# Performance work log

Measured on AMD Instinct MI355X. Metric: run time of the kernel, lower is better.

The kernel has to match this reference:

```python
import jax, jax.numpy as jnp
import numpy as np

N_ROWS = 4_194_304  # batch rows
N_LAYERS = 30


def setup_inputs() -> dict:
    key = jax.random.key(0)
    k1, k2, k3, k4, k5 = jax.random.split(key, 5)
    x1 = jax.random.normal(k1, (N_ROWS, 1), dtype=jnp.float32)
    x2 = jax.random.normal(k2, (N_ROWS, 5), dtype=jnp.float32)
    # Per-layer params stacked: Linear(5->1) weight [1,5] + bias [1]; Linear(1->5, no bias) weight [5,1]
    W1 = jax.random.normal(k3, (N_LAYERS, 1, 5), dtype=jnp.float32) * (1.0 / np.sqrt(5.0))
    b1 = jax.random.normal(k4, (N_LAYERS, 1), dtype=jnp.float32) * (1.0 / np.sqrt(5.0))
    W2 = jax.random.normal(k5, (N_LAYERS, 5, 1), dtype=jnp.float32)
    return {"x1": x1, "x2": x2, "W1": W1, "b1": b1, "W2": W2}


def reference(x1, x2, W1, b1, W2):
    # Chain of 30 UpDownDoubleResNetBlock blocks:
    #   x1 = x1 + relu(x2) @ W1^T + b1   (Linear(5,1) with bias)
    #   x2 = x2 + relu(x1) @ W2^T        (Linear(1,5) no bias)
    def step(carry, params):
        h1, h2 = carry
        w1, bb1, w2 = params  # [1,5], [1], [5,1]
        h1 = h1 + jax.nn.relu(h2) @ w1.T + bb1  # [N,1]
        h2 = h2 + jax.nn.relu(h1) @ w2.T        # [N,5]
        return (h1, h2), None

    (x1, x2), _ = jax.lax.scan(step, (x1, x2), (W1, b1, W2))
    return (x1, x2)
```

## Files before the change

kernel.cpp:

```cpp
#include <hip/hip_runtime.h>

#define NL 30

typedef float f32x2 __attribute__((ext_vector_type(2)));

static __device__ __forceinline__ f32x2 splat2(float v) { return (f32x2){v, v}; }

__global__ __launch_bounds__(256) void drn_kernel(
    const float* __restrict__ x1, const float* __restrict__ x2,
    const float* __restrict__ W1, const float* __restrict__ b1,
    const float* __restrict__ W2,
    float* __restrict__ o1, float* __restrict__ o2, int nrows)
{
    long t = (long)blockIdx.x * blockDim.x + threadIdx.x;
    long row0 = t * 4;
    if (row0 >= nrows) return;

    float4 h1v = *(const float4*)(x1 + row0);
    float xs[20];
    {
        const float4* px2 = (const float4*)(x2 + row0 * 5);
        #pragma unroll
        for (int i = 0; i < 5; ++i) ((float4*)xs)[i] = px2[i];
    }

    f32x2 h1p[2] = { (f32x2){h1v.x, h1v.y}, (f32x2){h1v.z, h1v.w} };
    f32x2 h2[5][2];
    #pragma unroll
    for (int j = 0; j < 5; ++j) {
        h2[j][0] = (f32x2){xs[0 * 5 + j], xs[1 * 5 + j]};
        h2[j][1] = (f32x2){xs[2 * 5 + j], xs[3 * 5 + j]};
    }

    const f32x2 zero = splat2(0.0f);

    for (int l = 0; l < NL; ++l) {
        float w1r[5], w2r[5];
        #pragma unroll
        for (int j = 0; j < 5; ++j) w1r[j] = W1[l * 5 + j];
        float bb = b1[l];
        #pragma unroll
        for (int j = 0; j < 5; ++j) w2r[j] = W2[l * 5 + j];

        #pragma unroll
        for (int p = 0; p < 2; ++p) {
            f32x2 s = h1p[p] + splat2(bb);
            #pragma unroll
            for (int j = 0; j < 5; ++j)
                s += __builtin_elementwise_max(h2[j][p], zero) * splat2(w1r[j]);
            h1p[p] = s;
            f32x2 rh = __builtin_elementwise_max(s, zero);
            #pragma unroll
            for (int j = 0; j < 5; ++j)
                h2[j][p] += rh * splat2(w2r[j]);
        }
    }

    float ys[20];
    #pragma unroll
    for (int j = 0; j < 5; ++j) {
        ys[0 * 5 + j] = h2[j][0].x;
        ys[1 * 5 + j] = h2[j][0].y;
        ys[2 * 5 + j] = h2[j][1].x;
        ys[3 * 5 + j] = h2[j][1].y;
    }

    *(float4*)(o1 + row0) = make_float4(h1p[0].x, h1p[0].y, h1p[1].x, h1p[1].y);
    float4* po2 = (float4*)(o2 + row0 * 5);
    #pragma unroll
    for (int i = 0; i < 5; ++i) po2[i] = ((float4*)ys)[i];
}

extern "C" void kernel_launch(void* const* d_in, const int* in_sizes, int n_in,
                              void* d_out, int out_size, void* d_ws, size_t ws_size,
                              hipStream_t stream) {
    const float* x1 = (const float*)d_in[0];
    const float* x2 = (const float*)d_in[1];
    const float* W1 = (const float*)d_in[2];
    const float* b1 = (const float*)d_in[3];
    const float* W2 = (const float*)d_in[4];
    int nrows = in_sizes[0];
    float* o1 = (float*)d_out;
    float* o2 = (float*)d_out + nrows;

    int nthreads = nrows / 4;
    int block = 256;
    int grid = (nthreads + block - 1) / block;
    drn_kernel<<<grid, block, 0, stream>>>(x1, x2, W1, b1, W2, o1, o2, nrows);
}
```

Measured before the change: 206.9 us.

## Process eight rows per thread with pre-splatted packed params and explicit FMAs

Each thread now handles eight rows instead of four, which halves the thread count and spreads each per-layer weight load over more work. A small pre-kernel packs W1, b1 and W2 into duplicated float2 pairs in workspace, so the main loop can feed packed FMA directly without splat moves. The inner math uses explicit elementwise FMA, and the layer loop is fully unrolled. The cost is higher register pressure (40+ live floats) and lower occupancy, plus an extra kernel launch.

```diff
diff --git a/kernel.cpp b/kernel.cpp
--- a/kernel.cpp
+++ b/kernel.cpp
@@ -4,71 +4,92 @@
 
 typedef float f32x2 __attribute__((ext_vector_type(2)));
 
-static __device__ __forceinline__ f32x2 splat2(float v) { return (f32x2){v, v}; }
+__global__ void pack_params(const float* __restrict__ W1,
+                            const float* __restrict__ b1,
+                            const float* __restrict__ W2,
+                            f32x2* __restrict__ pw) {
+    int i = blockIdx.x * blockDim.x + threadIdx.x;
+    if (i >= NL * 11) return;
+    int l = i / 11, k = i % 11;
+    float v;
+    if (k < 5)       v = W1[l * 5 + k];
+    else if (k == 5) v = b1[l];
+    else             v = W2[l * 5 + (k - 6)];
+    pw[i] = (f32x2){v, v};
+}
 
 __global__ __launch_bounds__(256) void drn_kernel(
     const float* __restrict__ x1, const float* __restrict__ x2,
-    const float* __restrict__ W1, const float* __restrict__ b1,
-    const float* __restrict__ W2,
+    const f32x2* __restrict__ pw,
     float* __restrict__ o1, float* __restrict__ o2, int nrows)
 {
     long t = (long)blockIdx.x * blockDim.x + threadIdx.x;
-    long row0 = t * 4;
+    long row0 = t * 8;
     if (row0 >= nrows) return;
 
-    float4 h1v = *(const float4*)(x1 + row0);
-    float xs[20];
-    {
-        const float4* px2 = (const float4*)(x2 + row0 * 5);
+    float h1s[8];
+    const float4* px1 = (const float4*)(x1 + row0);
+    *(float4*)&h1s[0] = px1[0];
+    *(float4*)&h1s[4] = px1[1];
+    float xs[40];
+    const float4* px2 = (const float4*)(x2 + row0 * 5);
+    #pragma unroll
+    for (int i = 0; i < 10; ++i) ((float4*)xs)[i] = px2[i];
+
+    f32x2 h1p[4];
+    f32x2 h2[5][4];
+    #pragma unroll
+    for (int p = 0; p < 4; ++p) {
+        h1p[p] = (f32x2){h1s[2 * p], h1s[2 * p + 1]};
         #pragma unroll
-        for (int i = 0; i < 5; ++i) ((float4*)xs)[i] = px2[i];
+        for (int j = 0; j < 5; ++j)
+            h2[j][p] = (f32x2){xs[(2 * p) * 5 + j], xs[(2 * p + 1) * 5 + j]};
     }
 
-    f32x2 h1p[2] = { (f32x2){h1v.x, h1v.y}, (f32x2){h1v.z, h1v.w} };
-    f32x2 h2[5][2];
+    const f32x2 zero = (f32x2){0.0f, 0.0f};
+
     #pragma unroll
-    for (int j = 0; j < 5; ++j) {
-        h2[j][0] = (f32x2){xs[0 * 5 + j], xs[1 * 5 + j]};
-        h2[j][1] = (f32x2){xs[2 * 5 + j], xs[3 * 5 + j]};
-    }
-
-    const f32x2 zero = splat2(0.0f);
-
     for (int l = 0; l < NL; ++l) {
-        float w1r[5], w2r[5];
+        const f32x2* P = pw + l * 11;
+        f32x2 w1d[5], w2d[5];
         #pragma unroll
-        for (int j = 0; j < 5; ++j) w1r[j] = W1[l * 5 + j];
-        float bb = b1[l];
+        for (int j = 0; j < 5; ++j) w1d[j] = P[j];
+        f32x2 bd = P[5];
         #pragma unroll
-        for (int j = 0; j < 5; ++j) w2r[j] = W2[l * 5 + j];
+        for (int j = 0; j < 5; ++j) w2d[j] = P[6 + j];
 
         #pragma unroll
-        for (int p = 0; p < 2; ++p) {
-            f32x2 s = h1p[p] + splat2(bb);
+        for (int p = 0; p < 4; ++p) {
+            f32x2 s = h1p[p] + bd;
             #pragma unroll
             for (int j = 0; j < 5; ++j)
-                s += __builtin_elementwise_max(h2[j][p], zero) * splat2(w1r[j]);
+                s = __builtin_elementwise_fma(
+                        __builtin_elementwise_max(h2[j][p], zero), w1d[j], s);
             h1p[p] = s;
             f32x2 rh = __builtin_elementwise_max(s, zero);
             #pragma unroll
             for (int j = 0; j < 5; ++j)
-                h2[j][p] += rh * splat2(w2r[j]);
+                h2[j][p] = __builtin_elementwise_fma(rh, w2d[j], h2[j][p]);
         }
     }
 
-    float ys[20];
+    float ys[40];
     #pragma unroll
-    for (int j = 0; j < 5; ++j) {
-        ys[0 * 5 + j] = h2[j][0].x;
-        ys[1 * 5 + j] = h2[j][0].y;
-        ys[2 * 5 + j] = h2[j][1].x;
-        ys[3 * 5 + j] = h2[j][1].y;
+    for (int p = 0; p < 4; ++p) {
+        h1s[2 * p]     = h1p[p].x;
+        h1s[2 * p + 1] = h1p[p].y;
+        #pragma unroll
+        for (int j = 0; j < 5; ++j) {
+            ys[(2 * p) * 5 + j]     = h2[j][p].x;
+            ys[(2 * p + 1) * 5 + j] = h2[j][p].y;
+        }
     }
-
-    *(float4*)(o1 + row0) = make_float4(h1p[0].x, h1p[0].y, h1p[1].x, h1p[1].y);
+    float4* po1 = (float4*)(o1 + row0);
+    po1[0] = *(float4*)&h1s[0];
+    po1[1] = *(float4*)&h1s[4];
     float4* po2 = (float4*)(o2 + row0 * 5);
     #pragma unroll
-    for (int i = 0; i < 5; ++i) po2[i] = ((float4*)ys)[i];
+    for (int i = 0; i < 10; ++i) po2[i] = ((float4*)ys)[i];
 }
 
 extern "C" void kernel_launch(void* const* d_in, const int* in_sizes, int n_in,
@@ -82,9 +103,12 @@
     int nrows = in_sizes[0];
     float* o1 = (float*)d_out;
     float* o2 = (float*)d_out + nrows;
+    f32x2* pw = (f32x2*)d_ws;
 
-    int nthreads = nrows / 4;
+    pack_params<<<2, 256, 0, stream>>>(W1, b1, W2, pw);
+
+    int nthreads = nrows / 8;
     int block = 256;
     int grid = (nthreads + block - 1) / block;
-    drn_kernel<<<grid, block, 0, stream>>>(x1, x2, W1, b1, W2, o1, o2, nrows);
+    drn_kernel<<<grid, block, 0, stream>>>(x1, x2, pw, o1, o2, nrows);
 }
```

Measured after the change: 208.6 us. Within noise of the previous version (+0.9%).
